# Optimization experiments

Hardware: AMD Instinct MI355X
Metric: run time of the kernel (lower is better)

## Reference

```python
import jax, jax.numpy as jnp
import numpy as np

THRESHOLD = 0.5
PSI_ZONE = 0.1


def dequantize_ternary(w, threshold=THRESHOLD, psi_zone=PSI_ZONE):
    """Faithful reproduction of TernaryTensor.from_float followed by to_float.

    Branch order matches the original code:
      v > threshold        -> +1
      v < -threshold       -> -1
      |v| < psi_zone       -> 0
      otherwise (PSI)      -> (v + threshold) / (2 * threshold)  (stored psi_prob)
    """
    psi_val = (w + threshold) / (2.0 * threshold)
    return jnp.where(
        w > threshold, 1.0,
        jnp.where(
            w < -threshold, -1.0,
            jnp.where(jnp.abs(w) < psi_zone, 0.0, psi_val),
        ),
    ).astype(w.dtype)


def setup_inputs() -> dict:
    key = jax.random.key(0)
    k_x, k_w = jax.random.split(key)
    batch, in_features, out_features = 8192, 4096, 4096
    x = jax.random.normal(k_x, (batch, in_features), dtype=jnp.float32)
    # original: torch.randn(out, in) * 0.1
    weight_float = jax.random.normal(k_w, (out_features, in_features), dtype=jnp.float32) * 0.1
    bias = jnp.zeros((out_features,), dtype=jnp.float32)
    return {"x": x, "weight_float": weight_float, "bias": bias}


def reference(x, weight_float, bias):
    w = dequantize_ternary(weight_float)  # [out, in]
    return jnp.matmul(x, w.T) + bias      # [batch, out]
```

## Files before the change

### kernel.cpp

```cpp
#include <hip/hip_runtime.h>
#include <stdint.h>

#define THRESH 0.5f
#define PSI 0.1f

typedef short bfrag_t __attribute__((ext_vector_type(8)));
typedef float f32x16 __attribute__((ext_vector_type(16)));
typedef unsigned short u16x8 __attribute__((ext_vector_type(8)));

#define GLD16(gsrc, ldst)                                                                \
    __builtin_amdgcn_global_load_lds((const __attribute__((address_space(1))) void*)(gsrc), \
                                     (__attribute__((address_space(3))) void*)(ldst),       \
                                     16, 0, 0)

#define WAITVM(n) asm volatile("s_waitcnt vmcnt(" #n ")" ::: "memory")
#define BAR()                                  \
    do {                                       \
        asm volatile("" ::: "memory");         \
        __builtin_amdgcn_s_barrier();          \
        asm volatile("" ::: "memory");         \
    } while (0)

__device__ __forceinline__ float dequant(float v) {
    if (v > THRESH) return 1.0f;
    if (v < -THRESH) return -1.0f;
    if (fabsf(v) < PSI) return 0.0f;
    return (v + THRESH) / (2.0f * THRESH);
}

__device__ __forceinline__ unsigned short f2bf(float f) {
    unsigned int u = __float_as_uint(f);
    u += 0x7FFFu + ((u >> 16) & 1u);
    return (unsigned short)(u >> 16);
}

template <bool DO_DEQUANT>
__global__ void pack_kernel(const float* __restrict__ src, unsigned short* __restrict__ dst, int K) {
    __shared__ char lsm[16384];
    const int t   = threadIdx.x;
    const int nkc = K >> 8;
    const int b   = blockIdx.x / nkc;
    const int kc  = blockIdx.x % nkc;
    const int k0  = kc << 8;
    const int r   = t >> 3;
    const int j   = t & 7;

    const float4* s4 = (const float4*)(src + (size_t)((b << 5) + r) * K + k0 + (j << 5));
    float4 f[8];
#pragma unroll
    for (int i = 0; i < 8; ++i) f[i] = s4[i];

#pragma unroll
    for (int gi = 0; gi < 4; ++gi) {
        float4 lo = f[2 * gi], hi4 = f[2 * gi + 1];
        u16x8 o;
        if (DO_DEQUANT) {
            o[0] = f2bf(dequant(lo.x));  o[1] = f2bf(dequant(lo.y));
            o[2] = f2bf(dequant(lo.z));  o[3] = f2bf(dequant(lo.w));
            o[4] = f2bf(dequant(hi4.x)); o[5] = f2bf(dequant(hi4.y));
            o[6] = f2bf(dequant(hi4.z)); o[7] = f2bf(dequant(hi4.w));
        } else {
            o[0] = f2bf(lo.x);  o[1] = f2bf(lo.y);  o[2] = f2bf(lo.z);  o[3] = f2bf(lo.w);
            o[4] = f2bf(hi4.x); o[5] = f2bf(hi4.y); o[6] = f2bf(hi4.z); o[7] = f2bf(hi4.w);
        }
        const int S_rel = 2 * j + (gi >> 1);
        const int slot  = ((gi & 1) << 5) + r;
        *(u16x8*)(lsm + S_rel * 1024 + slot * 16) = o;
    }
    __syncthreads();

    unsigned short* gdst = dst + (((size_t)b * (K >> 4) + (kc << 4)) << 9) + (size_t)t * 32;
#pragma unroll
    for (int i = 0; i < 4; ++i)
        *(u16x8*)(gdst + i * 8) = *(const u16x8*)(lsm + t * 64 + i * 16);
}


__device__ __forceinline__ bfrag_t rdfrag32(const char* halfBase, int band, int ks, int l16) {
    return *(const bfrag_t*)(halfBase + (band << 11) + (ks << 10) + l16);
}

__device__ __forceinline__ void mfma_half(f32x16 (&acc)[4][2], int mbase,
                                          const bfrag_t (&a)[2][2], const bfrag_t (&b)[2][2]) {
#pragma unroll
    for (int ks = 0; ks < 2; ++ks)
#pragma unroll
        for (int mi = 0; mi < 2; ++mi)
#pragma unroll
            for (int nn = 0; nn < 2; ++nn)
                acc[mbase + mi][nn] = __builtin_amdgcn_mfma_f32_32x32x16_bf16(
                    a[mi][ks], b[nn][ks], acc[mbase + mi][nn], 0, 0, 0);
}

__global__ __launch_bounds__(512, 2) void gemm256_kernel(
        const unsigned short* __restrict__ Ap,
        const unsigned short* __restrict__ Bp,
        const float* __restrict__ bias,
        float* __restrict__ C,
        int M, int N, int K) {
    __shared__ unsigned short lds[65536];
    char* ldsB = (char*)lds;

    const int t    = threadIdx.x;
    const int w    = t >> 6;
    const int l    = t & 63;
    const int wr   = w >> 2;
    const int wc   = w & 3;
    const int lr32 = l & 31;
    const int hi   = l >> 5;
    const int l16  = l << 4;

    const int nwg = gridDim.x;
    int bid = blockIdx.x;
    if ((nwg & 7) == 0) bid = (bid & 7) * (nwg >> 3) + (bid >> 3);
    const int nbn  = N >> 8;
    const int brow = (bid / nbn) << 8;
    const int bcol = (bid % nbn) << 8;

    const int Kc = K >> 4;
    const char* pA = (const char*)Ap + (((size_t)(((brow >> 5) + w) * (size_t)Kc)) << 10) + l16;
    const char* pB = (const char*)Bp + (((size_t)(((bcol >> 5) + w) * (size_t)Kc)) << 10) + l16;
    const int c16a = w * 2 + 0, c16b = w * 2 + 1;

#define STAGE_A(buf, half, kE)                                                              \
    do {                                                                                    \
        const size_t so_ = ((size_t)(((kE) >> 4) + (half) * 2)) << 10;                      \
        GLD16(pA + so_,        ldsB + (buf) * 65536 + (half) * 16384 + c16a * 1024);        \
        GLD16(pA + so_ + 1024, ldsB + (buf) * 65536 + (half) * 16384 + c16b * 1024);        \
    } while (0)
#define STAGE_B(buf, half, kE)                                                              \
    do {                                                                                    \
        const size_t so_ = ((size_t)(((kE) >> 4) + (half) * 2)) << 10;                      \
        GLD16(pB + so_,        ldsB + (buf) * 65536 + 32768 + (half) * 16384 + c16a * 1024);\
        GLD16(pB + so_ + 1024, ldsB + (buf) * 65536 + 32768 + (half) * 16384 + c16b * 1024);\
    } while (0)

    f32x16 acc[4][2];
#pragma unroll
    for (int m = 0; m < 4; ++m)
#pragma unroll
        for (int n = 0; n < 2; ++n)
#pragma unroll
            for (int r = 0; r < 16; ++r)
                acc[m][n][r] = 0.f;

    const int NT = K >> 6;
    const int wrB4 = wr << 2;
    const int wcB2 = wc << 1;
    const int wrBase = wr << 7;
    const int wcBase = wc << 6;

    {
        const int k1 = (NT > 1) ? 64 : 0;
        STAGE_A(0, 0, 0); STAGE_B(0, 0, 0);
        STAGE_A(0, 1, 0); STAGE_B(0, 1, 0);
        STAGE_A(1, 0, k1); STAGE_B(1, 0, k1);
        WAITVM(4);
        BAR();
    }

    for (int tt = 0; tt < NT; ++tt) {
        const int X = tt & 1, Y = X ^ 1;
        const char* aH0 = ldsB + X * 65536;
        const char* aH1 = aH0 + 16384;
        const char* bH0 = aH0 + 32768;
        const char* bH1 = aH0 + 49152;
        int t1 = tt + 1; if (t1 >= NT) t1 -= NT;
        int t2 = tt + 2; if (t2 >= NT) t2 -= NT;
        const int kY1 = t1 << 6;
        const int kX2 = t2 << 6;

        bfrag_t a[2][2], b[2][2];

#pragma unroll
        for (int mi = 0; mi < 2; ++mi)
#pragma unroll
            for (int ks = 0; ks < 2; ++ks)
                a[mi][ks] = rdfrag32(aH0, wrB4 + mi, ks, l16);
#pragma unroll
        for (int nn = 0; nn < 2; ++nn)
#pragma unroll
            for (int ks = 0; ks < 2; ++ks)
                b[nn][ks] = rdfrag32(bH0, wcB2 + nn, ks, l16);
        STAGE_A(Y, 1, kY1);
        BAR();
        __builtin_amdgcn_s_setprio(1);
        mfma_half(acc, 0, a, b);
        __builtin_amdgcn_s_setprio(0);
        BAR();

#pragma unroll
        for (int mi = 0; mi < 2; ++mi)
#pragma unroll
            for (int ks = 0; ks < 2; ++ks)
                a[mi][ks] = rdfrag32(aH0, wrB4 + 2 + mi, ks, l16);
        STAGE_B(Y, 1, kY1);
        BAR();
        __builtin_amdgcn_s_setprio(1);
        mfma_half(acc, 2, a, b);
        __builtin_amdgcn_s_setprio(0);
        WAITVM(8);
        BAR();

#pragma unroll
        for (int mi = 0; mi < 2; ++mi)
#pragma unroll
            for (int ks = 0; ks < 2; ++ks)
                a[mi][ks] = rdfrag32(aH1, wrB4 + mi, ks, l16);
#pragma unroll
        for (int nn = 0; nn < 2; ++nn)
#pragma unroll
            for (int ks = 0; ks < 2; ++ks)
                b[nn][ks] = rdfrag32(bH1, wcB2 + nn, ks, l16);
        STAGE_A(X, 0, kX2);
        BAR();
        __builtin_amdgcn_s_setprio(1);
        mfma_half(acc, 0, a, b);
        __builtin_amdgcn_s_setprio(0);
        BAR();

#pragma unroll
        for (int mi = 0; mi < 2; ++mi)
#pragma unroll
            for (int ks = 0; ks < 2; ++ks)
                a[mi][ks] = rdfrag32(aH1, wrB4 + 2 + mi, ks, l16);
        STAGE_B(X, 0, kX2);
        BAR();
        __builtin_amdgcn_s_setprio(1);
        mfma_half(acc, 2, a, b);
        __builtin_amdgcn_s_setprio(0);
        WAITVM(8);
        BAR();
    }

    WAITVM(0);

    float bv[2];
#pragma unroll
    for (int nn = 0; nn < 2; ++nn) bv[nn] = bias[bcol + wcBase + nn * 32 + lr32];
#pragma unroll
    for (int mm = 0; mm < 4; ++mm) {
#pragma unroll
        for (int nn = 0; nn < 2; ++nn) {
            const int gc = bcol + wcBase + nn * 32 + lr32;
#pragma unroll
            for (int reg = 0; reg < 16; ++reg) {
                const int row = (reg & 3) + 8 * (reg >> 2) + 4 * hi;
                C[(size_t)(brow + wrBase + mm * 32 + row) * N + gc] = acc[mm][nn][reg] + bv[nn];
            }
        }
    }
    (void)M;
#undef STAGE_A
#undef STAGE_B
}

__global__ void gemm_fallback_kernel(const float* __restrict__ X, const float* __restrict__ W,
                                     const float* __restrict__ bias, float* __restrict__ C,
                                     int M, int N, int K) {
    __shared__ float sX[16][17];
    __shared__ float sW[16][17];
    const int tx = threadIdx.x & 15;
    const int ty = threadIdx.x >> 4;
    const int row = blockIdx.y * 16 + ty;
    const int colBase = blockIdx.x * 16;
    const int col = colBase + tx;
    float acc = 0.f;
    for (int k0 = 0; k0 < K; k0 += 16) {
        sX[ty][tx] = (row < M && k0 + tx < K) ? X[(size_t)row * K + k0 + tx] : 0.f;
        const int wrow = colBase + ty;
        sW[ty][tx] = (wrow < N && k0 + tx < K) ? dequant(W[(size_t)wrow * K + k0 + tx]) : 0.f;
        __syncthreads();
#pragma unroll
        for (int kk = 0; kk < 16; ++kk)
            acc += sX[ty][kk] * sW[tx][kk];
        __syncthreads();
    }
    if (row < M && col < N)
        C[(size_t)row * N + col] = acc + bias[col];
}

extern "C" void kernel_launch(void* const* d_in, const int* in_sizes, int n_in,
                              void* d_out, int out_size, void* d_ws, size_t ws_size,
                              hipStream_t stream) {
    const float* x    = (const float*)d_in[0];
    const float* w    = (const float*)d_in[1];
    const float* bias = (const float*)d_in[2];
    float* out        = (float*)d_out;

    const int N = in_sizes[2];
    const int K = in_sizes[1] / N;
    const int M = in_sizes[0] / K;

    const size_t need = ((size_t)M * K + (size_t)N * K) * sizeof(unsigned short);
    const bool fast = (ws_size >= need) && (M % 256 == 0) && (N % 256 == 0) &&
                      (K % 256 == 0);

    if (fast) {
        unsigned short* xp = (unsigned short*)d_ws;
        unsigned short* wp = xp + (size_t)M * K;
        pack_kernel<false><<<dim3((M / 32) * (K / 256)), dim3(256), 0, stream>>>(x, xp, K);
        pack_kernel<true ><<<dim3((N / 32) * (K / 256)), dim3(256), 0, stream>>>(w, wp, K);
        gemm256_kernel<<<dim3((M / 256) * (N / 256)), dim3(512), 0, stream>>>(xp, wp, bias, out, M, N, K);
    } else {
        dim3 g((N + 15) / 16, (M + 15) / 16);
        gemm_fallback_kernel<<<g, dim3(256), 0, stream>>>(x, w, bias, out, M, N, K);
    }
    (void)n_in; (void)out_size;
}
```

Before: 286.2 us.

## Restructure GEMM main loop to load whole K-tile fragments once per iteration

Each iteration now reads every A and B fragment for both K halves from LDS into registers up front, then runs two 16-MFMA bursts. Between the bursts it waits on LDS reads, takes one barrier and issues all four global-to-LDS stages for tile tt+2 into the same buffer. This cuts the barriers per iteration from eight to two and drops the interleaved half-tile staging. The cost is more live fragment registers, which could lower occupancy under launch_bounds(512,2), and coarser overlap of global loads with compute.

```diff
diff --git a/kernel.cpp b/kernel.cpp
--- a/kernel.cpp
+++ b/kernel.cpp
@@ -14,6 +14,7 @@
                                      16, 0, 0)
 
 #define WAITVM(n) asm volatile("s_waitcnt vmcnt(" #n ")" ::: "memory")
+#define WAITLGKM0() asm volatile("s_waitcnt lgkmcnt(0)" ::: "memory")
 #define BAR()                                  \
     do {                                       \
         asm volatile("" ::: "memory");         \
@@ -80,16 +81,16 @@
     return *(const bfrag_t*)(halfBase + (band << 11) + (ks << 10) + l16);
 }
 
-__device__ __forceinline__ void mfma_half(f32x16 (&acc)[4][2], int mbase,
-                                          const bfrag_t (&a)[2][2], const bfrag_t (&b)[2][2]) {
+__device__ __forceinline__ void mfma16(f32x16 (&acc)[4][2],
+                                       const bfrag_t (&a)[4][2], const bfrag_t (&b)[2][2]) {
 #pragma unroll
     for (int ks = 0; ks < 2; ++ks)
 #pragma unroll
-        for (int mi = 0; mi < 2; ++mi)
+        for (int mi = 0; mi < 4; ++mi)
 #pragma unroll
             for (int nn = 0; nn < 2; ++nn)
-                acc[mbase + mi][nn] = __builtin_amdgcn_mfma_f32_32x32x16_bf16(
-                    a[mi][ks], b[nn][ks], acc[mbase + mi][nn], 0, 0, 0);
+                acc[mi][nn] = __builtin_amdgcn_mfma_f32_32x32x16_bf16(
+                    a[mi][ks], b[nn][ks], acc[mi][nn], 0, 0, 0);
 }
 
 __global__ __launch_bounds__(512, 2) void gemm256_kernel(
@@ -152,83 +153,58 @@
 
     {
         const int k1 = (NT > 1) ? 64 : 0;
-        STAGE_A(0, 0, 0); STAGE_B(0, 0, 0);
-        STAGE_A(0, 1, 0); STAGE_B(0, 1, 0);
-        STAGE_A(1, 0, k1); STAGE_B(1, 0, k1);
-        WAITVM(4);
+        STAGE_A(0, 0, 0);  STAGE_B(0, 0, 0);  STAGE_A(0, 1, 0);  STAGE_B(0, 1, 0);
+        STAGE_A(1, 0, k1); STAGE_B(1, 0, k1); STAGE_A(1, 1, k1); STAGE_B(1, 1, k1);
+        WAITVM(8);
         BAR();
     }
 
     for (int tt = 0; tt < NT; ++tt) {
-        const int X = tt & 1, Y = X ^ 1;
+        const int X = tt & 1;
         const char* aH0 = ldsB + X * 65536;
         const char* aH1 = aH0 + 16384;
         const char* bH0 = aH0 + 32768;
         const char* bH1 = aH0 + 49152;
-        int t1 = tt + 1; if (t1 >= NT) t1 -= NT;
         int t2 = tt + 2; if (t2 >= NT) t2 -= NT;
-        const int kY1 = t1 << 6;
         const int kX2 = t2 << 6;
 
-        bfrag_t a[2][2], b[2][2];
-
-#pragma unroll
-        for (int mi = 0; mi < 2; ++mi)
-#pragma unroll
-            for (int ks = 0; ks < 2; ++ks)
-                a[mi][ks] = rdfrag32(aH0, wrB4 + mi, ks, l16);
+        bfrag_t a0[4][2], b0[2][2], a1[4][2], b1[2][2];
+
+#pragma unroll
+        for (int mi = 0; mi < 4; ++mi)
+#pragma unroll
+            for (int ks = 0; ks < 2; ++ks)
+                a0[mi][ks] = rdfrag32(aH0, wrB4 + mi, ks, l16);
 #pragma unroll
         for (int nn = 0; nn < 2; ++nn)
 #pragma unroll
             for (int ks = 0; ks < 2; ++ks)
-                b[nn][ks] = rdfrag32(bH0, wcB2 + nn, ks, l16);
-        STAGE_A(Y, 1, kY1);
+                b0[nn][ks] = rdfrag32(bH0, wcB2 + nn, ks, l16);
+#pragma unroll
+        for (int nn = 0; nn < 2; ++nn)
+#pragma unroll
+            for (int ks = 0; ks < 2; ++ks)
+                b1[nn][ks] = rdfrag32(bH1, wcB2 + nn, ks, l16);
+#pragma unroll
+        for (int mi = 0; mi < 4; ++mi)
+#pragma unroll
+            for (int ks = 0; ks < 2; ++ks)
+                a1[mi][ks] = rdfrag32(aH1, wrB4 + mi, ks, l16);
+
+        __builtin_amdgcn_s_setprio(1);
+        mfma16(acc, a0, b0);
+        __builtin_amdgcn_s_setprio(0);
+
+        WAITLGKM0();
         BAR();
+
+        STAGE_A(X, 0, kX2); STAGE_B(X, 0, kX2);
+        STAGE_A(X, 1, kX2); STAGE_B(X, 1, kX2);
+
         __builtin_amdgcn_s_setprio(1);
-        mfma_half(acc, 0, a, b);
+        mfma16(acc, a1, b1);
         __builtin_amdgcn_s_setprio(0);
-        BAR();
-
-#pragma unroll
-        for (int mi = 0; mi < 2; ++mi)
-#pragma unroll
-            for (int ks = 0; ks < 2; ++ks)
-                a[mi][ks] = rdfrag32(aH0, wrB4 + 2 + mi, ks, l16);
-        STAGE_B(Y, 1, kY1);
-        BAR();
-        __builtin_amdgcn_s_setprio(1);
-        mfma_half(acc, 2, a, b);
-        __builtin_amdgcn_s_setprio(0);
-        WAITVM(8);
-        BAR();
-
-#pragma unroll
-        for (int mi = 0; mi < 2; ++mi)
-#pragma unroll
-            for (int ks = 0; ks < 2; ++ks)
-                a[mi][ks] = rdfrag32(aH1, wrB4 + mi, ks, l16);
-#pragma unroll
-        for (int nn = 0; nn < 2; ++nn)
-#pragma unroll
-            for (int ks = 0; ks < 2; ++ks)
-                b[nn][ks] = rdfrag32(bH1, wcB2 + nn, ks, l16);
-        STAGE_A(X, 0, kX2);
-        BAR();
-        __builtin_amdgcn_s_setprio(1);
-        mfma_half(acc, 0, a, b);
-        __builtin_amdgcn_s_setprio(0);
-        BAR();
-
-#pragma unroll
-        for (int mi = 0; mi < 2; ++mi)
-#pragma unroll
-            for (int ks = 0; ks < 2; ++ks)
-                a[mi][ks] = rdfrag32(aH1, wrB4 + 2 + mi, ks, l16);
-        STAGE_B(X, 0, kX2);
-        BAR();
-        __builtin_amdgcn_s_setprio(1);
-        mfma_half(acc, 2, a, b);
-        __builtin_amdgcn_s_setprio(0);
+
         WAITVM(8);
         BAR();
     }
```

Measured after the change: 292.2 us. +2.1%, slower.
